# Optimization experiments

Measured on AMD Instinct MI355X. Metric: run time of the kernel, lower is better.

## Reference

```python
import jax, jax.numpy as jnp
import numpy as np

B, LQ, LK = 128, 512, 512
QS, KS, AS = 256, 256, 64


def setup_inputs() -> dict:
    key = jax.random.key(0)
    ks = jax.random.split(key, 7)
    s = 0.05
    return {
        "queries": jax.random.normal(ks[0], (B, LQ, QS), dtype=jnp.float32),
        "keys": jax.random.normal(ks[1], (B, LK, KS), dtype=jnp.float32),
        "w_relation": jax.random.normal(ks[2], (QS, KS), dtype=jnp.float32) * s,
        "W_q": jax.random.normal(ks[3], (QS, AS), dtype=jnp.float32) * s,
        "W_k": jax.random.normal(ks[4], (KS, AS), dtype=jnp.float32) * s,
        "W_q_att": jax.random.normal(ks[5], (AS, 1), dtype=jnp.float32) * s,
        "W_k_att": jax.random.normal(ks[6], (AS, 1), dtype=jnp.float32) * s,
    }


def reference(queries, keys, w_relation, W_q, W_k, W_q_att, W_k_att):
    # relation_scores: [B, Lq, Lk]
    rel = jnp.tanh(jnp.einsum("bqd,de,bke->bqk", queries, w_relation, keys))
    q_proj = jnp.einsum("bqd,da->bqa", queries, W_q)   # [B, Lq, A]
    k_proj = jnp.einsum("bkd,da->bka", keys, W_k)      # [B, Lk, A]
    q_att_score = jnp.tanh(q_proj + jnp.einsum("bqk,bka->bqa", rel, k_proj))
    k_att_score = jnp.tanh(k_proj + jnp.einsum("bqk,bqa->bka", rel, q_proj))
    # softmax over the sequence dim (dim=1)
    q_att_w = jax.nn.softmax(q_att_score @ W_q_att, axis=1)  # [B, Lq, 1]
    k_att_w = jax.nn.softmax(k_att_score @ W_k_att, axis=1)  # [B, Lk, 1]
    weighted_queries = q_att_w * queries
    weighted_keys = k_att_w * keys
    return (weighted_queries, weighted_keys, q_att_w, k_att_w)
```

## Files before the change

### kernel.cpp

```cpp
#include <hip/hip_runtime.h>
#include <math.h>


#define SEQ 512
#define DIM 256
#define ADIM 64
#define OUT_QATT ((size_t)33554432)

using hfrag = __attribute__((ext_vector_type(8))) _Float16;
using s4 = __attribute__((ext_vector_type(4))) short;
using f4 = __attribute__((ext_vector_type(4))) float;
typedef unsigned int u32;

__device__ __forceinline__ void gl_lds16(const short* g, short* l) {
  __builtin_amdgcn_global_load_lds((const __attribute__((address_space(1))) u32*)g,
                                   (__attribute__((address_space(3))) u32*)l, 16, 0, 0);
}

__device__ __forceinline__ short f2h(float x) {
  _Float16 h = (_Float16)x;
  return __builtin_bit_cast(short, h);
}
__device__ __forceinline__ float h2f(short s) {
  return (float)__builtin_bit_cast(_Float16, s);
}
__device__ __forceinline__ float tanhf_fast(float x) {
  float e = __expf(2.0f * x);
  return 1.0f - 2.0f / (e + 1.0f);
}


template <int KTOT>
__device__ __forceinline__ void core128(const short* __restrict__ A,
                                        const short* __restrict__ Bt,
                                        short* sA, short* sB, f4 acc[4][4]) {
  const int t = threadIdx.x;
  const int lane = t & 63, wave = t >> 6;
  const int wm = (wave & 1) << 6, wn = (wave >> 1) << 6;
  const int l15 = lane & 15, qd = lane >> 4;
  const int srow = t >> 3, scol = (t & 7) << 3;
  for (int k0 = 0; k0 < KTOT; k0 += 64) {
#pragma unroll
    for (int i = 0; i < 4; i++) {
      const int row = srow + (i << 5);
      const int gcol = k0 + (scol ^ ((row & 7) << 3));
      gl_lds16(&A[(size_t)row * KTOT + gcol], &sA[t * 8 + i * 2048]);
      gl_lds16(&Bt[(size_t)row * KTOT + gcol], &sB[t * 8 + i * 2048]);
    }
    __syncthreads();
#pragma unroll
    for (int ks = 0; ks < 2; ks++) {
      hfrag af[4], bg[4];
      const int kk = (ks << 5) + (qd << 3);
#pragma unroll
      for (int i = 0; i < 4; i++) {
        const int ar = wm + (i << 4) + l15;
        const int br = wn + (i << 4) + l15;
        af[i] = *(const hfrag*)&sA[(ar << 6) + (kk ^ ((ar & 7) << 3))];
        bg[i] = *(const hfrag*)&sB[(br << 6) + (kk ^ ((br & 7) << 3))];
      }
#pragma unroll
      for (int i = 0; i < 4; i++)
#pragma unroll
        for (int j = 0; j < 4; j++)
          acc[i][j] = __builtin_amdgcn_mfma_f32_16x16x32_f16(af[i], bg[j], acc[i][j], 0, 0, 0);
    }
    __syncthreads();
  }
}

template <int KTOT>
__device__ __forceinline__ void core64(const short* __restrict__ A,
                                       const short* __restrict__ Bt,
                                       short* sA, short* sB, f4 acc[4][2]) {
  const int t = threadIdx.x;
  const int lane = t & 63, wave = t >> 6;
  const int wm = (wave & 1) << 6, wn = (wave >> 1) << 5;
  const int l15 = lane & 15, qd = lane >> 4;
  const int srow = t >> 3, scol = (t & 7) << 3;
  for (int k0 = 0; k0 < KTOT; k0 += 64) {
#pragma unroll
    for (int i = 0; i < 4; i++) {
      const int row = srow + (i << 5);
      const int gcol = k0 + (scol ^ ((row & 7) << 3));
      gl_lds16(&A[(size_t)row * KTOT + gcol], &sA[t * 8 + i * 2048]);
      if (i < 2) gl_lds16(&Bt[(size_t)row * KTOT + gcol], &sB[t * 8 + i * 2048]);
    }
    __syncthreads();
#pragma unroll
    for (int ks = 0; ks < 2; ks++) {
      hfrag af[4], bg[2];
      const int kk = (ks << 5) + (qd << 3);
#pragma unroll
      for (int i = 0; i < 4; i++) {
        const int ar = wm + (i << 4) + l15;
        af[i] = *(const hfrag*)&sA[(ar << 6) + (kk ^ ((ar & 7) << 3))];
      }
#pragma unroll
      for (int j = 0; j < 2; j++) {
        const int br = wn + (j << 4) + l15;
        bg[j] = *(const hfrag*)&sB[(br << 6) + (kk ^ ((br & 7) << 3))];
      }
#pragma unroll
      for (int i = 0; i < 4; i++)
#pragma unroll
        for (int j = 0; j < 2; j++)
          acc[i][j] = __builtin_amdgcn_mfma_f32_16x16x32_f16(af[i], bg[j], acc[i][j], 0, 0, 0);
    }
    __syncthreads();
  }
}


__global__ __launch_bounds__(256) void cvt_kernel(const float* __restrict__ Q,
                                                  const float* __restrict__ K,
                                                  const float* __restrict__ wrel,
                                                  const float* __restrict__ Wq,
                                                  const float* __restrict__ Wk,
                                                  short* __restrict__ Qh, short* __restrict__ Kh,
                                                  short* __restrict__ wrelT,
                                                  short* __restrict__ WqT,
                                                  short* __restrict__ WkT) {
  const int bid = blockIdx.x;
  if (bid < 32768) {
    const size_t g = ((size_t)bid << 8) + threadIdx.x;
    const int side = (int)(g >> 22);
    const size_t loc = g & 4194303;
    const float4 v = ((const float4*)(side ? K : Q))[loc];
    s4 o;
    o[0] = f2h(v.x); o[1] = f2h(v.y); o[2] = f2h(v.z); o[3] = f2h(v.w);
    *(s4*)&(side ? Kh : Qh)[loc << 2] = o;
  } else {
    const int b2 = bid - 32768;
    if (b2 < 64) {
      const int i = (b2 << 8) + threadIdx.x;
#pragma unroll
      for (int u = 0; u < 4; u++) {
        const int idx = (i << 2) + u;
        const int e = idx >> 8, d = idx & 255;
        wrelT[idx] = f2h(wrel[(d << 8) + e]);
      }
    } else if (b2 < 72) {
      const int i = ((b2 - 64) << 8) + threadIdx.x;
#pragma unroll
      for (int u = 0; u < 8; u++) {
        const int idx = (i << 3) + u;
        const int a = idx >> 8, d = idx & 255;
        WqT[idx] = f2h(Wq[(d << 6) + a]);
      }
    } else if (b2 < 80) {
      const int i = ((b2 - 72) << 8) + threadIdx.x;
#pragma unroll
      for (int u = 0; u < 8; u++) {
        const int idx = (i << 3) + u;
        const int a = idx >> 8, d = idx & 255;
        WkT[idx] = f2h(Wk[(d << 6) + a]);
      }
    }
  }
}

__global__ __launch_bounds__(256) void proj_kernel(const short* __restrict__ Qh,
                                                   const short* __restrict__ Kh,
                                                   const short* __restrict__ WqT,
                                                   const short* __restrict__ WkT,
                                                   short* __restrict__ qp, short* __restrict__ kp,
                                                   short* __restrict__ qpT, short* __restrict__ kpT) {
  __shared__ short sA[8192];
  __shared__ short sB[4096];
  const int which = blockIdx.y;
  const short* A = which ? Kh : Qh;
  const short* Bt = which ? WkT : WqT;
  short* P = which ? kp : qp;
  short* PT = which ? kpT : qpT;
  const int m0 = blockIdx.x << 7;
  f4 acc[4][2];
  const f4 fz = {0.f, 0.f, 0.f, 0.f};
#pragma unroll
  for (int i = 0; i < 4; i++)
#pragma unroll
    for (int j = 0; j < 2; j++) acc[i][j] = fz;
  core64<256>(A + (size_t)m0 * 256, Bt, sA, sB, acc);
  const int lane = threadIdx.x & 63, wave = threadIdx.x >> 6;
  const int wm = (wave & 1) << 6, wn = (wave >> 1) << 5;
  const int l15 = lane & 15, qd = lane >> 4;
#pragma unroll
  for (int i = 0; i < 4; i++)
#pragma unroll
    for (int j = 0; j < 2; j++) {
      s4 pack;
      const int gm0 = m0 + wm + (i << 4) + (qd << 2);
      const int a = wn + (j << 4) + l15;
#pragma unroll
      for (int r = 0; r < 4; r++) {
        pack[r] = f2h(acc[i][j][r]);
        P[(size_t)(gm0 + r) * ADIM + a] = pack[r];
      }
      const int bb = gm0 >> 9, ql = gm0 & 511;
      *(s4*)&PT[((size_t)bb * ADIM + a) * SEQ + ql] = pack;
    }
}

__global__ __launch_bounds__(256) void qw_kernel(const short* __restrict__ Qh,
                                                 const short* __restrict__ WrT,
                                                 short* __restrict__ qw) {
  __shared__ short sA[8192];
  __shared__ short sB[8192];
  const int m0 = blockIdx.x << 7, n0 = blockIdx.y << 7;
  f4 acc[4][4];
  const f4 fz = {0.f, 0.f, 0.f, 0.f};
#pragma unroll
  for (int i = 0; i < 4; i++)
#pragma unroll
    for (int j = 0; j < 4; j++) acc[i][j] = fz;
  core128<256>(Qh + (size_t)m0 * 256, WrT + (size_t)n0 * 256, sA, sB, acc);
  const int lane = threadIdx.x & 63, wave = threadIdx.x >> 6;
  const int wm = (wave & 1) << 6, wn = (wave >> 1) << 6;
  const int l15 = lane & 15, qd = lane >> 4;
#pragma unroll
  for (int i = 0; i < 4; i++)
#pragma unroll
    for (int j = 0; j < 4; j++)
#pragma unroll
      for (int r = 0; r < 4; r++) {
        const int row = m0 + wm + (i << 4) + (qd << 2) + r;
        const int col = n0 + wn + (j << 4) + l15;
        qw[(size_t)row * 256 + col] = f2h(acc[i][j][r]);
      }
}

__global__ __launch_bounds__(256) void fused_kernel(const short* __restrict__ qw,
                                                    const short* __restrict__ Kh,
                                                    const short* __restrict__ qpT,
                                                    const short* __restrict__ kpT,
                                                    const short* __restrict__ qp,
                                                    const float* __restrict__ Wqa,
                                                    float* __restrict__ kpart,
                                                    float* __restrict__ qlog) {
  __shared__ short smem[32768];
  short* sA = smem;
  short* sB = smem + 8192;
  short* tile = smem;
  short* tileT = smem + 16384;
  const int mt = blockIdx.x, b = blockIdx.y;
  const int t = threadIdx.x;
  const int lane = t & 63, wave = t >> 6;
  const int l15 = lane & 15, qd = lane >> 4;
  const int wm = (wave & 1) << 6, wn = (wave >> 1) << 6;
  const int rbase = wave << 5;
  const f4 fz = {0.f, 0.f, 0.f, 0.f};

  f4 qacc[2][4];
#pragma unroll
  for (int i2 = 0; i2 < 2; i2++)
#pragma unroll
    for (int j2 = 0; j2 < 4; j2++) qacc[i2][j2] = fz;

  const short* kpT_b = kpT + ((size_t)b * ADIM) * SEQ;
  const short* qpT_b = qpT + ((size_t)b * ADIM) * SEQ;

  for (int n0 = 0; n0 < 4; n0++) {
    f4 acc[4][4];
#pragma unroll
    for (int i = 0; i < 4; i++)
#pragma unroll
      for (int j = 0; j < 4; j++) acc[i][j] = fz;
    core128<256>(qw + ((size_t)b * SEQ + mt * 128) * 256,
                 Kh + ((size_t)b * SEQ + n0 * 128) * 256, sA, sB, acc);
#pragma unroll
    for (int i = 0; i < 4; i++)
#pragma unroll
      for (int j = 0; j < 4; j++) {
        const int row0 = wm + (i << 4) + (qd << 2);
        const int col = wn + (j << 4) + l15;
        s4 pack;
#pragma unroll
        for (int r = 0; r < 4; r++) {
          const short h = f2h(tanhf_fast(acc[i][j][r]));
          pack[r] = h;
          const int row = row0 + r;
          tile[(row << 7) + (col ^ ((row & 7) << 3))] = h;
        }
        *(s4*)&tileT[(col << 7) + (row0 ^ ((col & 7) << 3))] = pack;
      }
    __syncthreads();
    f4 kacc[2][4];
#pragma unroll
    for (int i2 = 0; i2 < 2; i2++)
#pragma unroll
      for (int j2 = 0; j2 < 4; j2++) kacc[i2][j2] = fz;
#pragma unroll
    for (int ks = 0; ks < 4; ks++) {
      const int kkk = (ks << 5) + (qd << 3);
      hfrag aq[2], ak[2], bq[4], bk[4];
#pragma unroll
      for (int i2 = 0; i2 < 2; i2++) {
        const int ar = rbase + (i2 << 4) + l15;
        aq[i2] = *(const hfrag*)&tile[(ar << 7) + (kkk ^ ((ar & 7) << 3))];
        ak[i2] = *(const hfrag*)&tileT[(ar << 7) + (kkk ^ ((ar & 7) << 3))];
      }
#pragma unroll
      for (int j2 = 0; j2 < 4; j2++) {
        const int a = (j2 << 4) + l15;
        bq[j2] = *(const hfrag*)&kpT_b[(size_t)a * SEQ + (n0 << 7) + kkk];
        bk[j2] = *(const hfrag*)&qpT_b[(size_t)a * SEQ + (mt << 7) + kkk];
      }
#pragma unroll
      for (int i2 = 0; i2 < 2; i2++)
#pragma unroll
        for (int j2 = 0; j2 < 4; j2++) {
          qacc[i2][j2] = __builtin_amdgcn_mfma_f32_16x16x32_f16(aq[i2], bq[j2], qacc[i2][j2], 0, 0, 0);
          kacc[i2][j2] = __builtin_amdgcn_mfma_f32_16x16x32_f16(ak[i2], bk[j2], kacc[i2][j2], 0, 0, 0);
        }
    }
#pragma unroll
    for (int i2 = 0; i2 < 2; i2++)
#pragma unroll
      for (int j2 = 0; j2 < 4; j2++) {
        const int krow = (n0 << 7) + rbase + (i2 << 4) + (qd << 2);
        const int a = (j2 << 4) + l15;
#pragma unroll
        for (int r = 0; r < 4; r++)
          kpart[((((size_t)b << 2) + mt) * SEQ + krow + r) * ADIM + a] = kacc[i2][j2][r];
      }
    __syncthreads();
  }
  float p[2][4];
#pragma unroll
  for (int i2 = 0; i2 < 2; i2++)
#pragma unroll
    for (int r = 0; r < 4; r++) p[i2][r] = 0.f;
#pragma unroll
  for (int i2 = 0; i2 < 2; i2++)
#pragma unroll
    for (int r = 0; r < 4; r++) {
      const int q = (mt << 7) + rbase + (i2 << 4) + (qd << 2) + r;
      const size_t gq = (size_t)b * SEQ + q;
#pragma unroll
      for (int j2 = 0; j2 < 4; j2++) {
        const int a = (j2 << 4) + l15;
        p[i2][r] += tanhf_fast(h2f(qp[gq * ADIM + a]) + qacc[i2][j2][r]) * Wqa[a];
      }
    }
#pragma unroll
  for (int off = 8; off; off >>= 1)
#pragma unroll
    for (int i2 = 0; i2 < 2; i2++)
#pragma unroll
      for (int r = 0; r < 4; r++) p[i2][r] += __shfl_down(p[i2][r], off, 16);
  if (l15 == 0) {
#pragma unroll
    for (int i2 = 0; i2 < 2; i2++)
#pragma unroll
      for (int r = 0; r < 4; r++) {
        const int q = (mt << 7) + rbase + (i2 << 4) + (qd << 2) + r;
        qlog[(size_t)b * SEQ + q] = p[i2][r];
      }
  }
}

__global__ __launch_bounds__(256) void klog_kernel(const float* __restrict__ kpart,
                                                   const short* __restrict__ kp,
                                                   const float* __restrict__ Wka,
                                                   float* __restrict__ klog) {
  const int half = blockIdx.x, b = blockIdx.y;
  const int t = threadIdx.x, a = t & 63, wave = t >> 6;
  const float w = Wka[a];
  const int kbase = (half << 8) + (wave << 6);
  const size_t pb = ((size_t)b << 2) * SEQ * ADIM;
  for (int it = 0; it < 64; it++) {
    const int k = kbase + it;
    const size_t base = pb + (size_t)k * ADIM + a;
    float s = kpart[base] + kpart[base + (size_t)SEQ * ADIM] +
              kpart[base + (size_t)2 * SEQ * ADIM] + kpart[base + (size_t)3 * SEQ * ADIM];
    s = tanhf_fast(s + h2f(kp[((size_t)b * SEQ + k) * ADIM + a])) * w;
#pragma unroll
    for (int off = 32; off; off >>= 1) s += __shfl_xor(s, off);
    if (a == 0) klog[(size_t)b * SEQ + k] = s;
  }
}

__global__ __launch_bounds__(256) void softmax_kernel(const float* __restrict__ qlog,
                                                      const float* __restrict__ klog,
                                                      float* __restrict__ out) {
  const int bx = blockIdx.x;
  const int side = bx >> 7;
  const int b = bx & 127;
  const float* lg = (side ? klog : qlog) + (size_t)b * SEQ;
  float* o = out + OUT_QATT + (size_t)side * (128 * SEQ) + (size_t)b * SEQ;
  const int t = threadIdx.x;
  float v0 = lg[t];
  float v1 = lg[t + 256];
  float m = fmaxf(v0, v1);
#pragma unroll
  for (int off = 32; off; off >>= 1) m = fmaxf(m, __shfl_xor(m, off));
  __shared__ float sm[4], ss[4];
  const int w = t >> 6, l = t & 63;
  if (l == 0) sm[w] = m;
  __syncthreads();
  m = fmaxf(fmaxf(sm[0], sm[1]), fmaxf(sm[2], sm[3]));
  float e0 = expf(v0 - m), e1 = expf(v1 - m);
  float s = e0 + e1;
#pragma unroll
  for (int off = 32; off; off >>= 1) s += __shfl_xor(s, off);
  if (l == 0) ss[w] = s;
  __syncthreads();
  s = ss[0] + ss[1] + ss[2] + ss[3];
  float inv = 1.0f / s;
  o[t] = e0 * inv;
  o[t + 256] = e1 * inv;
}

__global__ __launch_bounds__(256) void weight_kernel(const float* __restrict__ queries,
                                                     const float* __restrict__ keys,
                                                     float* __restrict__ out) {
  const size_t g = (size_t)blockIdx.x * 256 + threadIdx.x;
  const int side = (int)(g >> 22);
  const size_t loc = g & 4194303;
  const size_t row = loc >> 6;
  const float* aw = out + OUT_QATT + (size_t)side * (128 * SEQ);
  const float4* src = (const float4*)(side ? keys : queries);
  const float w = aw[row];
  float4 v = src[loc];
  float4 r = {v.x * w, v.y * w, v.z * w, v.w * w};
  ((float4*)out)[g] = r;
}

extern "C" void kernel_launch(void* const* d_in, const int* in_sizes, int n_in,
                              void* d_out, int out_size, void* d_ws, size_t ws_size,
                              hipStream_t stream) {
  const float* queries = (const float*)d_in[0];
  const float* keys = (const float*)d_in[1];
  const float* w_rel = (const float*)d_in[2];
  const float* W_q = (const float*)d_in[3];
  const float* W_k = (const float*)d_in[4];
  const float* W_qa = (const float*)d_in[5];
  const float* W_ka = (const float*)d_in[6];
  float* out = (float*)d_out;

  short* Qh = (short*)d_ws;
  short* Kh = Qh + 16777216;
  short* qp = Kh + 16777216;
  short* kp = qp + 4194304;
  float* qlog = (float*)(kp + 4194304);
  float* klog = qlog + 65536;

  char* ob = (char*)d_out;
  short* qw_s = (short*)ob;
  float* kpart = (float*)(ob + 33554432);
  short* qpT = (short*)(ob + 100663296);
  short* kpT = (short*)(ob + 109051904);
  short* wrelT = (short*)(ob + 117440512);
  short* WqT = (short*)(ob + 117571584);
  short* WkT = (short*)(ob + 117604352);

  cvt_kernel<<<32848, 256, 0, stream>>>(queries, keys, w_rel, W_q, W_k, Qh, Kh, wrelT, WqT, WkT);
  proj_kernel<<<dim3(512, 2), 256, 0, stream>>>(Qh, Kh, WqT, WkT, qp, kp, qpT, kpT);
  qw_kernel<<<dim3(512, 2), 256, 0, stream>>>(Qh, wrelT, qw_s);
  fused_kernel<<<dim3(4, 128), 256, 0, stream>>>(qw_s, Kh, qpT, kpT, qp, W_qa, kpart, qlog);
  klog_kernel<<<dim3(2, 128), 256, 0, stream>>>(kpart, kp, W_ka, klog);
  softmax_kernel<<<256, 256, 0, stream>>>(qlog, klog, out);
  weight_kernel<<<32768, 256, 0, stream>>>(queries, keys, out);
}
```

Measured before the change: 450.8 us.

## Split fused relation kernel into independent query/key side kernels, drop kpart reduction

Replaces the fused kernel, which computed both the query-side and key-side contributions per 128-row query tile and wrote key partial sums, with one side_kernel launched over a z dimension of 2. Each block owns 64 rows of one side, keeps its A tile resident in LDS, streams the other side's B tiles, and computes that side's full logit directly. This removes the kpart global round trip and the separate klog_kernel, and raises the grid from 512 to 2048 blocks with an occupancy hint. In exchange the relation GEMM (tanh(qw·K^T)) is computed twice, once per side, which doubles that MFMA work.

```diff
diff --git a/kernel.cpp b/kernel.cpp
--- a/kernel.cpp
+++ b/kernel.cpp
@@ -229,154 +229,136 @@
       }
 }
 
-__global__ __launch_bounds__(256) void fused_kernel(const short* __restrict__ qw,
-                                                    const short* __restrict__ Kh,
-                                                    const short* __restrict__ qpT,
-                                                    const short* __restrict__ kpT,
-                                                    const short* __restrict__ qp,
-                                                    const float* __restrict__ Wqa,
-                                                    float* __restrict__ kpart,
-                                                    float* __restrict__ qlog) {
-  __shared__ short smem[32768];
-  short* sA = smem;
-  short* sB = smem + 8192;
-  short* tile = smem;
-  short* tileT = smem + 16384;
-  const int mt = blockIdx.x, b = blockIdx.y;
+__global__ __launch_bounds__(256, 4) void side_kernel(const short* __restrict__ qw,
+                                                      const short* __restrict__ Kh,
+                                                      const short* __restrict__ qpT,
+                                                      const short* __restrict__ kpT,
+                                                      const short* __restrict__ qp,
+                                                      const short* __restrict__ kp,
+                                                      const float* __restrict__ Wqa,
+                                                      const float* __restrict__ Wka,
+                                                      float* __restrict__ qlog,
+                                                      float* __restrict__ klog) {
+  __shared__ short sA[16384];
+  __shared__ short sB[8192];
+  const int sideK = blockIdx.z;
+  const short* Asrc = sideK ? Kh : qw;
+  const short* Bsrc = sideK ? qw : Kh;
+  const short* pT = sideK ? qpT : kpT;
+  const short* prow = sideK ? kp : qp;
+  const float* Watt = sideK ? Wka : Wqa;
+  float* logit = sideK ? klog : qlog;
+
+  const int tt = blockIdx.x;
+  const int b = blockIdx.y;
   const int t = threadIdx.x;
   const int lane = t & 63, wave = t >> 6;
   const int l15 = lane & 15, qd = lane >> 4;
-  const int wm = (wave & 1) << 6, wn = (wave >> 1) << 6;
-  const int rbase = wave << 5;
+  const int wm = (wave & 1) << 5, wn = (wave >> 1) << 6;
   const f4 fz = {0.f, 0.f, 0.f, 0.f};
 
-  f4 qacc[2][4];
-#pragma unroll
-  for (int i2 = 0; i2 < 2; i2++)
-#pragma unroll
-    for (int j2 = 0; j2 < 4; j2++) qacc[i2][j2] = fz;
-
-  const short* kpT_b = kpT + ((size_t)b * ADIM) * SEQ;
-  const short* qpT_b = qpT + ((size_t)b * ADIM) * SEQ;
+  {
+    const short* Ag = Asrc + ((size_t)b * SEQ + tt * 64) * DIM;
+    const int chunk = t & 31;
+    const int rb = t >> 5;
+#pragma unroll
+    for (int i = 0; i < 8; i++) {
+      const int row = (i << 3) + rb;
+      const int gcol = (chunk << 3) ^ ((row & 7) << 3);
+      gl_lds16(&Ag[(size_t)row * DIM + gcol], &sA[(row << 8) + (chunk << 3)]);
+    }
+  }
+
+  f4 pacc[4];
+#pragma unroll
+  for (int j = 0; j < 4; j++) pacc[j] = fz;
+
+  const short* pT_b = pT + (size_t)b * ADIM * SEQ;
+  const int srow = t >> 3, scol = (t & 7) << 3;
 
   for (int n0 = 0; n0 < 4; n0++) {
-    f4 acc[4][4];
-#pragma unroll
-    for (int i = 0; i < 4; i++)
+    f4 acc[2][4];
+#pragma unroll
+    for (int i = 0; i < 2; i++)
 #pragma unroll
       for (int j = 0; j < 4; j++) acc[i][j] = fz;
-    core128<256>(qw + ((size_t)b * SEQ + mt * 128) * 256,
-                 Kh + ((size_t)b * SEQ + n0 * 128) * 256, sA, sB, acc);
-#pragma unroll
-    for (int i = 0; i < 4; i++)
+    const short* Bg = Bsrc + ((size_t)b * SEQ + n0 * 128) * DIM;
+    for (int k0 = 0; k0 < 256; k0 += 64) {
+#pragma unroll
+      for (int i = 0; i < 4; i++) {
+        const int row = srow + (i << 5);
+        const int gcol = k0 + (scol ^ ((row & 7) << 3));
+        gl_lds16(&Bg[(size_t)row * DIM + gcol], &sB[t * 8 + i * 2048]);
+      }
+      __syncthreads();
+#pragma unroll
+      for (int ks = 0; ks < 2; ks++) {
+        const int kkB = (ks << 5) + (qd << 3);
+        const int kkA = k0 + kkB;
+        hfrag af[2], bg[4];
+#pragma unroll
+        for (int i = 0; i < 2; i++) {
+          const int ar = wm + (i << 4) + l15;
+          af[i] = *(const hfrag*)&sA[(ar << 8) + (kkA ^ ((ar & 7) << 3))];
+        }
+#pragma unroll
+        for (int j = 0; j < 4; j++) {
+          const int br = wn + (j << 4) + l15;
+          bg[j] = *(const hfrag*)&sB[(br << 6) + (kkB ^ ((br & 7) << 3))];
+        }
+#pragma unroll
+        for (int i = 0; i < 2; i++)
+#pragma unroll
+          for (int j = 0; j < 4; j++)
+            acc[i][j] = __builtin_amdgcn_mfma_f32_16x16x32_f16(af[i], bg[j], acc[i][j], 0, 0, 0);
+      }
+      __syncthreads();
+    }
+#pragma unroll
+    for (int i = 0; i < 2; i++)
 #pragma unroll
       for (int j = 0; j < 4; j++) {
         const int row0 = wm + (i << 4) + (qd << 2);
         const int col = wn + (j << 4) + l15;
-        s4 pack;
 #pragma unroll
         for (int r = 0; r < 4; r++) {
-          const short h = f2h(tanhf_fast(acc[i][j][r]));
-          pack[r] = h;
           const int row = row0 + r;
-          tile[(row << 7) + (col ^ ((row & 7) << 3))] = h;
+          sB[(row << 7) + (col ^ ((row & 7) << 3))] = f2h(tanhf_fast(acc[i][j][r]));
         }
-        *(s4*)&tileT[(col << 7) + (row0 ^ ((col & 7) << 3))] = pack;
-      }
-    __syncthreads();
-    f4 kacc[2][4];
-#pragma unroll
-    for (int i2 = 0; i2 < 2; i2++)
-#pragma unroll
-      for (int j2 = 0; j2 < 4; j2++) kacc[i2][j2] = fz;
+      }
+    __syncthreads();
 #pragma unroll
     for (int ks = 0; ks < 4; ks++) {
       const int kkk = (ks << 5) + (qd << 3);
-      hfrag aq[2], ak[2], bq[4], bk[4];
-#pragma unroll
-      for (int i2 = 0; i2 < 2; i2++) {
-        const int ar = rbase + (i2 << 4) + l15;
-        aq[i2] = *(const hfrag*)&tile[(ar << 7) + (kkk ^ ((ar & 7) << 3))];
-        ak[i2] = *(const hfrag*)&tileT[(ar << 7) + (kkk ^ ((ar & 7) << 3))];
-      }
+      const int ar = (wave << 4) + l15;
+      const hfrag aq = *(const hfrag*)&sB[(ar << 7) + (kkk ^ ((ar & 7) << 3))];
 #pragma unroll
       for (int j2 = 0; j2 < 4; j2++) {
         const int a = (j2 << 4) + l15;
-        bq[j2] = *(const hfrag*)&kpT_b[(size_t)a * SEQ + (n0 << 7) + kkk];
-        bk[j2] = *(const hfrag*)&qpT_b[(size_t)a * SEQ + (mt << 7) + kkk];
-      }
-#pragma unroll
-      for (int i2 = 0; i2 < 2; i2++)
-#pragma unroll
-        for (int j2 = 0; j2 < 4; j2++) {
-          qacc[i2][j2] = __builtin_amdgcn_mfma_f32_16x16x32_f16(aq[i2], bq[j2], qacc[i2][j2], 0, 0, 0);
-          kacc[i2][j2] = __builtin_amdgcn_mfma_f32_16x16x32_f16(ak[i2], bk[j2], kacc[i2][j2], 0, 0, 0);
-        }
-    }
-#pragma unroll
-    for (int i2 = 0; i2 < 2; i2++)
-#pragma unroll
-      for (int j2 = 0; j2 < 4; j2++) {
-        const int krow = (n0 << 7) + rbase + (i2 << 4) + (qd << 2);
-        const int a = (j2 << 4) + l15;
-#pragma unroll
-        for (int r = 0; r < 4; r++)
-          kpart[((((size_t)b << 2) + mt) * SEQ + krow + r) * ADIM + a] = kacc[i2][j2][r];
-      }
-    __syncthreads();
-  }
-  float p[2][4];
-#pragma unroll
-  for (int i2 = 0; i2 < 2; i2++)
-#pragma unroll
-    for (int r = 0; r < 4; r++) p[i2][r] = 0.f;
-#pragma unroll
-  for (int i2 = 0; i2 < 2; i2++)
-#pragma unroll
-    for (int r = 0; r < 4; r++) {
-      const int q = (mt << 7) + rbase + (i2 << 4) + (qd << 2) + r;
-      const size_t gq = (size_t)b * SEQ + q;
-#pragma unroll
-      for (int j2 = 0; j2 < 4; j2++) {
-        const int a = (j2 << 4) + l15;
-        p[i2][r] += tanhf_fast(h2f(qp[gq * ADIM + a]) + qacc[i2][j2][r]) * Wqa[a];
-      }
+        const hfrag bq = *(const hfrag*)&pT_b[(size_t)a * SEQ + (n0 << 7) + kkk];
+        pacc[j2] = __builtin_amdgcn_mfma_f32_16x16x32_f16(aq, bq, pacc[j2], 0, 0, 0);
+      }
+    }
+    __syncthreads();
+  }
+
+  const int row_l = (wave << 4) + (qd << 2);
+  const size_t g0 = (size_t)b * SEQ + tt * 64 + row_l;
+  float p[4] = {0.f, 0.f, 0.f, 0.f};
+#pragma unroll
+  for (int r = 0; r < 4; r++)
+#pragma unroll
+    for (int j2 = 0; j2 < 4; j2++) {
+      const int a = (j2 << 4) + l15;
+      p[r] += tanhf_fast(h2f(prow[(g0 + r) * ADIM + a]) + pacc[j2][r]) * Watt[a];
     }
 #pragma unroll
   for (int off = 8; off; off >>= 1)
 #pragma unroll
-    for (int i2 = 0; i2 < 2; i2++)
-#pragma unroll
-      for (int r = 0; r < 4; r++) p[i2][r] += __shfl_down(p[i2][r], off, 16);
+    for (int r = 0; r < 4; r++) p[r] += __shfl_down(p[r], off, 16);
   if (l15 == 0) {
 #pragma unroll
-    for (int i2 = 0; i2 < 2; i2++)
-#pragma unroll
-      for (int r = 0; r < 4; r++) {
-        const int q = (mt << 7) + rbase + (i2 << 4) + (qd << 2) + r;
-        qlog[(size_t)b * SEQ + q] = p[i2][r];
-      }
-  }
-}
-
-__global__ __launch_bounds__(256) void klog_kernel(const float* __restrict__ kpart,
-                                                   const short* __restrict__ kp,
-                                                   const float* __restrict__ Wka,
-                                                   float* __restrict__ klog) {
-  const int half = blockIdx.x, b = blockIdx.y;
-  const int t = threadIdx.x, a = t & 63, wave = t >> 6;
-  const float w = Wka[a];
-  const int kbase = (half << 8) + (wave << 6);
-  const size_t pb = ((size_t)b << 2) * SEQ * ADIM;
-  for (int it = 0; it < 64; it++) {
-    const int k = kbase + it;
-    const size_t base = pb + (size_t)k * ADIM + a;
-    float s = kpart[base] + kpart[base + (size_t)SEQ * ADIM] +
-              kpart[base + (size_t)2 * SEQ * ADIM] + kpart[base + (size_t)3 * SEQ * ADIM];
-    s = tanhf_fast(s + h2f(kp[((size_t)b * SEQ + k) * ADIM + a])) * w;
-#pragma unroll
-    for (int off = 32; off; off >>= 1) s += __shfl_xor(s, off);
-    if (a == 0) klog[(size_t)b * SEQ + k] = s;
+    for (int r = 0; r < 4; r++) logit[g0 + r] = p[r];
   }
 }
 
@@ -447,7 +429,6 @@
 
   char* ob = (char*)d_out;
   short* qw_s = (short*)ob;
-  float* kpart = (float*)(ob + 33554432);
   short* qpT = (short*)(ob + 100663296);
   short* kpT = (short*)(ob + 109051904);
   short* wrelT = (short*)(ob + 117440512);
@@ -457,8 +438,7 @@
   cvt_kernel<<<32848, 256, 0, stream>>>(queries, keys, w_rel, W_q, W_k, Qh, Kh, wrelT, WqT, WkT);
   proj_kernel<<<dim3(512, 2), 256, 0, stream>>>(Qh, Kh, WqT, WkT, qp, kp, qpT, kpT);
   qw_kernel<<<dim3(512, 2), 256, 0, stream>>>(Qh, wrelT, qw_s);
-  fused_kernel<<<dim3(4, 128), 256, 0, stream>>>(qw_s, Kh, qpT, kpT, qp, W_qa, kpart, qlog);
-  klog_kernel<<<dim3(2, 128), 256, 0, stream>>>(kpart, kp, W_ka, klog);
+  side_kernel<<<dim3(8, 128, 2), 256, 0, stream>>>(qw_s, Kh, qpT, kpT, qp, kp, W_qa, W_ka, qlog, klog);
   softmax_kernel<<<256, 256, 0, stream>>>(qlog, klog, out);
   weight_kernel<<<32768, 256, 0, stream>>>(queries, keys, out);
 }
```

Result: no change. 442.8 us (-1.8%).
